# Kernel tuning notes

Measured on AMD Instinct MI355X. Metric: run time of the kernel, lower is better.

Reference implementation:

```python
import jax, jax.numpy as jnp
import numpy as np

N = 8192
FEAT = 3
TRIG = 2
SA = 2
H = 64
ACT = 3
NEG = -1.0e9
EPS = 1e-5


def setup_inputs() -> dict:
    key = jax.random.key(0)
    ks = jax.random.split(key, 24)
    s = 0.05
    node_features = jax.random.uniform(ks[0], (N, FEAT), dtype=jnp.float32)
    adj = jax.random.randint(ks[1], (N, N), 0, 2).astype(jnp.float32)
    # ensure self-loops so every row has at least one neighbor
    adj_matrix = jnp.maximum(adj, jnp.eye(N, dtype=jnp.float32))
    trigger_context = jax.random.uniform(ks[2], (TRIG,), dtype=jnp.float32)
    sa_priors = jax.random.normal(ks[3], (N, SA), dtype=jnp.float32)
    p = lambda k, sh: jax.random.normal(k, sh, dtype=jnp.float32) * s
    return {
        "node_features": node_features,
        "adj_matrix": adj_matrix,
        "trigger_context": trigger_context,
        "sa_priors": sa_priors,
        # node_encoder: Linear(5,64) -> ReLU -> Linear(64,64)
        "w1": p(ks[4], (FEAT + TRIG, H)), "b1": jnp.zeros((H,), jnp.float32),
        "w2": p(ks[5], (H, H)), "b2": jnp.zeros((H,), jnp.float32),
        "wq": p(ks[6], (H, H)), "bq": jnp.zeros((H,), jnp.float32),
        "wk": p(ks[7], (H, H)), "bk": jnp.zeros((H,), jnp.float32),
        "wg": p(ks[8], (TRIG, H)), "bg": jnp.zeros((H,), jnp.float32),
        "stateful_bias": jnp.zeros((1,), jnp.float32),
        "wm": p(ks[9], (H, H)), "bm": jnp.zeros((H,), jnp.float32),
        "ln_g": jnp.ones((H,), jnp.float32), "ln_b": jnp.zeros((H,), jnp.float32),
        "wa1": p(ks[10], (H + SA, H)), "ba1": jnp.zeros((H,), jnp.float32),
        "wa2": p(ks[11], (H, ACT)), "ba2": jnp.zeros((ACT,), jnp.float32),
    }


def reference(node_features, adj_matrix, trigger_context, sa_priors,
              w1, b1, w2, b2, wq, bq, wk, bk, wg, bg, stateful_bias,
              wm, bm, ln_g, ln_b, wa1, ba1, wa2, ba2):
    n = node_features.shape[0]
    trig = jnp.broadcast_to(trigger_context[None, :], (n, TRIG))
    x = jnp.concatenate([node_features, trig], axis=1)          # [N, 5]
    h = jax.nn.relu(x @ w1 + b1) @ w2 + b2                       # [N, H]
    q = h @ wq + bq
    k = h @ wk + bk
    scores = (q @ k.T) * (1.0 / np.sqrt(H))                      # [N, N]
    gate_factor = jnp.mean(jax.nn.sigmoid(trigger_context @ wg + bg))
    topo = jnp.where(adj_matrix == 0, jnp.float32(NEG), adj_matrix)
    is_stateful = node_features[:, 2]
    is_reactive = 1.0 - trigger_context[0]
    sb = jnp.outer(is_stateful, is_stateful) * (stateful_bias[0] * is_reactive)
    scores = scores * gate_factor + topo + sb
    attn = jax.nn.softmax(scores, axis=1)                        # [N, N]
    messages = h @ wm + bm
    aggregated = attn @ messages                                 # [N, H]
    z = h + aggregated
    mu = jnp.mean(z, axis=-1, keepdims=True)
    var = jnp.mean(jnp.square(z - mu), axis=-1, keepdims=True)
    emb = (z - mu) * jax.lax.rsqrt(var + EPS) * ln_g + ln_b      # LayerNorm
    ai = jnp.concatenate([emb, sa_priors], axis=1)               # [N, H+2]
    q_values = jax.nn.relu(ai @ wa1 + ba1) @ wa2 + ba2           # [N, 3]
    return q_values
```

## Files before the change

### kernel.cpp

```cpp
#include <hip/hip_runtime.h>
#include <hip/hip_bf16.h>
#include <math.h>

#define N 8192
#define EPSV 1e-05f
#define NSPLIT 32
#define CPS (N / NSPLIT)
#define NSTEP (CPS / 32)

typedef short bf16x8 __attribute__((ext_vector_type(8)));
typedef float f32x4 __attribute__((ext_vector_type(4)));
typedef float f32x16 __attribute__((ext_vector_type(16)));
typedef unsigned short u16;
typedef unsigned int u32;
typedef unsigned long long u64;

#define WS_SCAL 0
#define WS_H    64
#define WS_ST   (WS_H + N * 64)
#define WS_SBI  (WS_ST + N)
#define WS_DEN  (WS_SBI + N)
#define WS_AGG  (WS_DEN + N)
#define WS_F_END (WS_AGG + N * 64)
#define WU_BASE (WS_F_END * 2)
#define WU_QB (WU_BASE)
#define WU_KB (WU_BASE + N * 64)
#define WU_MB (WU_BASE + 2 * N * 64)
#define WU_MT (WU_BASE + 3 * N * 64)

static __device__ __forceinline__ u16 f2bf(float f) {
    __hip_bfloat16 h = __float2bfloat16(f);
    return *(u16*)&h;
}
static __device__ __forceinline__ u32 pk2(float a, float b) {
    return (u32)f2bf(a) | ((u32)f2bf(b) << 16);
}
static __device__ __forceinline__ bf16x8 mk8(u32 a, u32 b, u32 c, u32 d) {
    union { u32 u[4]; bf16x8 v; } x;
    x.u[0] = a; x.u[1] = b; x.u[2] = c; x.u[3] = d;
    return x.v;
}

__global__ void prep_k(const float* __restrict__ tc, const float* __restrict__ wg,
                       const float* __restrict__ bg, const float* __restrict__ sbias,
                       float* __restrict__ scal) {
    int j = threadIdx.x;
    float v = tc[0] * wg[j] + tc[1] * wg[64 + j] + bg[j];
    float g = 1.0f / (1.0f + __expf(-v));
    for (int off = 32; off; off >>= 1) g += __shfl_xor(g, off, 64);
    if (j == 0) {
        scal[0] = 0.125f * (g * (1.0f / 64.0f));
        scal[1] = sbias[0] * (1.0f - tc[0]);
    }
}

__global__ __launch_bounds__(256) void embed_k(
    const float* __restrict__ nf, const float* __restrict__ tc,
    const float* __restrict__ w1, const float* __restrict__ b1,
    const float* __restrict__ w2, const float* __restrict__ b2,
    const float* __restrict__ wq, const float* __restrict__ bq,
    const float* __restrict__ wk, const float* __restrict__ bk,
    const float* __restrict__ wm, const float* __restrict__ bm,
    float* __restrict__ ws)
{
    const int w = threadIdx.x >> 6, lane = threadIdx.x & 63;
    const int row = blockIdx.x * 4 + w;
    __shared__ float ts[4][64], hs[4][64];
    const float qscale = ws[WS_SCAL + 0];
    const float coef   = ws[WS_SCAL + 1];
    const float f0 = nf[row * 3], f1 = nf[row * 3 + 1], f2 = nf[row * 3 + 2];
    const float t0 = tc[0], t1 = tc[1];
    ws[WS_AGG + (size_t)row * 64 + lane] = 0.0f;
    float v = b1[lane];
    v = fmaf(f0, w1[lane], v);
    v = fmaf(f1, w1[64 + lane], v);
    v = fmaf(f2, w1[128 + lane], v);
    v = fmaf(t0, w1[192 + lane], v);
    v = fmaf(t1, w1[256 + lane], v);
    ts[w][lane] = fmaxf(v, 0.0f);
    __syncthreads();
    float hv = b2[lane];
    #pragma unroll 8
    for (int j = 0; j < 64; j++) hv = fmaf(ts[w][j], w2[j * 64 + lane], hv);
    hs[w][lane] = hv;
    ws[WS_H + row * 64 + lane] = hv;
    __syncthreads();
    float qv = bq[lane], kv = bk[lane], mv = bm[lane];
    #pragma unroll 4
    for (int j = 0; j < 64; j++) {
        const float hj = hs[w][j];
        qv = fmaf(hj, wq[j * 64 + lane], qv);
        kv = fmaf(hj, wk[j * 64 + lane], kv);
        mv = fmaf(hj, wm[j * 64 + lane], mv);
    }
    u16* wu = (u16*)ws;
    wu[WU_QB + row * 64 + lane] = f2bf(qv * qscale);
    wu[WU_KB + row * 64 + lane] = f2bf(kv);
    wu[WU_MB + row * 64 + lane] = f2bf(mv);
    if (lane == 0) {
        ws[WS_ST + row]  = f2;
        ws[WS_SBI + row] = f2 * coef;
        ws[WS_DEN + row] = 0.0f;
    }
}

__global__ __launch_bounds__(256) void transp_k(float* __restrict__ ws) {
    const u16* mb = (const u16*)ws + WU_MB;
    u16* mt = (u16*)ws + WU_MT;
    __shared__ __align__(16) u16 tile[64][72];
    const int i0 = blockIdx.x * 64;
    const int t = threadIdx.x;
    {
        const int r = t >> 2, cb = (t & 3) * 16;
        *(uint4*)&tile[r][cb]     = *(const uint4*)&mb[(size_t)(i0 + r) * 64 + cb];
        *(uint4*)&tile[r][cb + 8] = *(const uint4*)&mb[(size_t)(i0 + r) * 64 + cb + 8];
    }
    __syncthreads();
    const int c = t >> 2, rb = (t & 3) * 16;
    u16 tmp[16];
    #pragma unroll
    for (int i = 0; i < 16; i++) tmp[i] = tile[rb + i][c];
    *(uint4*)&mt[(size_t)c * N + i0 + rb]     = *(uint4*)&tmp[0];
    *(uint4*)&mt[(size_t)c * N + i0 + rb + 8] = *(uint4*)&tmp[8];
}

__global__ __launch_bounds__(512, 4) void attn_k(const float* __restrict__ adj,
                                                 float* __restrict__ ws)
{
    const int rb = blockIdx.x, sp = blockIdx.y;
    const int i0 = rb * 256, j0 = sp * CPS;
    const int tid = threadIdx.x;
    const int w = tid >> 6, lane = tid & 63;
    const int hi = lane >> 5, l31 = lane & 31;

    __shared__ __align__(16) u16 ks[256 * 64];
    __shared__ __align__(16) u16 ms[64 * 256];
    __shared__ u32 abit[256][9];
    __shared__ float stl[CPS];

    const u16* qb  = (const u16*)ws + WU_QB;
    const u16* kbp = (const u16*)ws + WU_KB;
    const u16* mtp = (const u16*)ws + WU_MT;

    {
        const size_t rowbase = (size_t)(i0 + w * 32) * N + j0;
        #pragma unroll 2
        for (int rb8 = 0; rb8 < 4; rb8++) {
            float v[8][4];
            #pragma unroll
            for (int i = 0; i < 8; i++)
                #pragma unroll
                for (int g = 0; g < 4; g++)
                    v[i][g] = adj[rowbase + (size_t)(rb8 * 8 + i) * N + g * 64 + lane];
            #pragma unroll
            for (int i = 0; i < 8; i++) {
                #pragma unroll
                for (int g = 0; g < 4; g++) {
                    const u64 m = __ballot(v[i][g] != 0.0f);
                    if (lane == 0) {
                        abit[w * 32 + rb8 * 8 + i][g * 2]     = (u32)m;
                        abit[w * 32 + rb8 * 8 + i][g * 2 + 1] = (u32)(m >> 32);
                    }
                }
            }
        }
    }

    #pragma unroll
    for (int i = 0; i < 4; i++) {
        const int id = tid + 512 * i;
        const int r = id >> 3, c = id & 7;
        const int off = r * 64 + (((c * 16) ^ ((r & 7) << 4)) >> 1);
        *(uint4*)&ks[off] = *(const uint4*)&kbp[(size_t)(j0 + r) * 64 + c * 8];
    }
    #pragma unroll
    for (int i = 0; i < 4; i++) {
        const int id = tid + 512 * i;
        const int r = id >> 5, c = id & 31;
        const int off = r * 256 + (((c * 16) ^ ((r & 7) << 4)) >> 1);
        *(uint4*)&ms[off] = *(const uint4*)&mtp[(size_t)r * N + j0 + c * 8];
    }
    if (tid < 256) stl[tid] = ws[WS_ST + j0 + tid];
    __syncthreads();

    const int q0 = i0 + w * 32;

    const u16* qr = qb + (size_t)(q0 + l31) * 64;
    bf16x8 qf[4];
    #pragma unroll
    for (int s = 0; s < 4; s++) qf[s] = *(const bf16x8*)&qr[s * 16 + hi * 8];

    const float sbr = ws[WS_SBI + q0 + l31];

    f32x16 acc[2];
    #pragma unroll
    for (int hb = 0; hb < 2; hb++)
        #pragma unroll
        for (int i = 0; i < 16; i++) acc[hb][i] = 0.0f;
    float den = 0.0f;

    #pragma unroll
    for (int s = 0; s < NSTEP; s++) {
        const int loc = s * 32;

        f32x16 d;
        #pragma unroll
        for (int i = 0; i < 16; i++) d[i] = 0.0f;
        __builtin_amdgcn_s_setprio(1);
        #pragma unroll
        for (int s4 = 0; s4 < 4; s4++) {
            const int R = loc + l31;
            const bf16x8 kf = *(const bf16x8*)
                &ks[R * 64 + (((s4 * 32 + hi * 16) ^ ((R & 7) << 4)) >> 1)];
            d = __builtin_amdgcn_mfma_f32_32x32x16_bf16(kf, qf[s4], d, 0, 0, 0);
        }
        __builtin_amdgcn_s_setprio(0);

        const u32 wq = abit[w * 32 + l31][s] >> (4 * hi);

        u32 wlo[4], whi[4];
        #pragma unroll
        for (int c2 = 0; c2 < 4; c2++) {
            const f32x4 sv = *(const f32x4*)&stl[loc + c2 * 8 + hi * 4];
            const float b0 = (float)((wq >> (8 * c2 + 0)) & 1u);
            const float b1 = (float)((wq >> (8 * c2 + 1)) & 1u);
            const float b2 = (float)((wq >> (8 * c2 + 2)) & 1u);
            const float b3 = (float)((wq >> (8 * c2 + 3)) & 1u);
            const float p0 = b0 * __expf(fmaf(sbr, sv[0], d[c2 * 4 + 0]));
            const float p1 = b1 * __expf(fmaf(sbr, sv[1], d[c2 * 4 + 1]));
            const float p2 = b2 * __expf(fmaf(sbr, sv[2], d[c2 * 4 + 2]));
            const float p3 = b3 * __expf(fmaf(sbr, sv[3], d[c2 * 4 + 3]));
            den += (p0 + p1) + (p2 + p3);
            wlo[c2] = pk2(p0, p1);
            whi[c2] = pk2(p2, p3);
        }

        bf16x8 pa[2];
        #pragma unroll
        for (int s2 = 0; s2 < 2; s2++) {
            const u32 xl0 = (u32)__shfl_xor((int)wlo[2 * s2],     32, 64);
            const u32 xh0 = (u32)__shfl_xor((int)whi[2 * s2],     32, 64);
            const u32 xl1 = (u32)__shfl_xor((int)wlo[2 * s2 + 1], 32, 64);
            const u32 xh1 = (u32)__shfl_xor((int)whi[2 * s2 + 1], 32, 64);
            const u32 f0 = hi ? xl1 : wlo[2 * s2];
            const u32 f1 = hi ? xh1 : whi[2 * s2];
            const u32 f2 = hi ? wlo[2 * s2 + 1] : xl0;
            const u32 f3 = hi ? whi[2 * s2 + 1] : xh0;
            pa[s2] = mk8(f0, f1, f2, f3);
        }

        __builtin_amdgcn_s_setprio(1);
        #pragma unroll
        for (int s2 = 0; s2 < 2; s2++) {
            #pragma unroll
            for (int hb = 0; hb < 2; hb++) {
                const int R2 = hb * 32 + l31;
                const bf16x8 mf = *(const bf16x8*)
                    &ms[R2 * 256 +
                        (((loc * 2 + s2 * 32 + hi * 16) ^ ((R2 & 7) << 4)) >> 1)];
                acc[hb] = __builtin_amdgcn_mfma_f32_32x32x16_bf16(pa[s2], mf, acc[hb], 0, 0, 0);
            }
        }
        __builtin_amdgcn_s_setprio(0);
    }

    den += __shfl_xor(den, 32, 64);
    if (hi == 0) unsafeAtomicAdd(&ws[WS_DEN + q0 + l31], den);

    float* aggp = ws + WS_AGG;
    #pragma unroll
    for (int hb = 0; hb < 2; hb++) {
        #pragma unroll
        for (int r = 0; r < 16; r++) {
            const int qv = (r & 3) + 8 * (r >> 2) + 4 * hi;
            unsafeAtomicAdd(&aggp[(size_t)(q0 + qv) * 64 + hb * 32 + l31],
                            acc[hb][r]);
        }
    }
}

__global__ __launch_bounds__(256) void final_k(
    const float* __restrict__ sa, const float* __restrict__ ln_g,
    const float* __restrict__ ln_b,
    const float* __restrict__ wa1, const float* __restrict__ ba1,
    const float* __restrict__ wa2, const float* __restrict__ ba2,
    const float* __restrict__ ws, float* __restrict__ out)
{
    const int w = threadIdx.x >> 6, lane = threadIdx.x & 63;
    const int row = blockIdx.x * 4 + w;
    __shared__ float es[4][64], hs2[4][64];
    const float a = ws[WS_AGG + (size_t)row * 64 + lane];
    const float d = ws[WS_DEN + row];
    const float z = ws[WS_H + row * 64 + lane] + a / d;
    float mu = z;
    for (int off = 32; off; off >>= 1) mu += __shfl_xor(mu, off, 64);
    mu *= (1.0f / 64.0f);
    const float zc = z - mu;
    float var = zc * zc;
    for (int off = 32; off; off >>= 1) var += __shfl_xor(var, off, 64);
    var *= (1.0f / 64.0f);
    const float emb = zc * rsqrtf(var + EPSV) * ln_g[lane] + ln_b[lane];
    es[w][lane] = emb;
    __syncthreads();
    const float sa0 = sa[row * 2], sa1 = sa[row * 2 + 1];
    float hv = ba1[lane];
    #pragma unroll 8
    for (int c = 0; c < 64; c++) hv = fmaf(es[w][c], wa1[c * 64 + lane], hv);
    hv = fmaf(sa0, wa1[64 * 64 + lane], hv);
    hv = fmaf(sa1, wa1[65 * 64 + lane], hv);
    hs2[w][lane] = fmaxf(hv, 0.0f);
    __syncthreads();
    if (lane < 3) {
        float o = ba2[lane];
        for (int u = 0; u < 64; u++) o = fmaf(hs2[w][u], wa2[u * 3 + lane], o);
        out[row * 3 + lane] = o;
    }
}

extern "C" void kernel_launch(void* const* d_in, const int* in_sizes, int n_in,
                              void* d_out, int out_size, void* d_ws, size_t ws_size,
                              hipStream_t stream)
{
    const float* nf  = (const float*)d_in[0];
    const float* adj = (const float*)d_in[1];
    const float* tc  = (const float*)d_in[2];
    const float* sa  = (const float*)d_in[3];
    const float* w1  = (const float*)d_in[4];
    const float* b1  = (const float*)d_in[5];
    const float* w2  = (const float*)d_in[6];
    const float* b2  = (const float*)d_in[7];
    const float* wq  = (const float*)d_in[8];
    const float* bq  = (const float*)d_in[9];
    const float* wk  = (const float*)d_in[10];
    const float* bk  = (const float*)d_in[11];
    const float* wg  = (const float*)d_in[12];
    const float* bg  = (const float*)d_in[13];
    const float* sb  = (const float*)d_in[14];
    const float* wm  = (const float*)d_in[15];
    const float* bm  = (const float*)d_in[16];
    const float* lng = (const float*)d_in[17];
    const float* lnb = (const float*)d_in[18];
    const float* wa1 = (const float*)d_in[19];
    const float* ba1 = (const float*)d_in[20];
    const float* wa2 = (const float*)d_in[21];
    const float* ba2 = (const float*)d_in[22];
    float* ws  = (float*)d_ws;
    float* out = (float*)d_out;

    prep_k<<<1, 64, 0, stream>>>(tc, wg, bg, sb, ws + WS_SCAL);
    embed_k<<<N / 4, 256, 0, stream>>>(nf, tc, w1, b1, w2, b2, wq, bq, wk, bk,
                                       wm, bm, ws);
    transp_k<<<N / 64, 256, 0, stream>>>(ws);
    attn_k<<<dim3(N / 256, NSPLIT), 512, 0, stream>>>(adj, ws);
    final_k<<<N / 4, 256, 0, stream>>>(sa, lng, lnb, wa1, ba1, wa2, ba2, ws, out);
}
```

Before: 450.6 us.

## Precompute adjacency bitmask in separate streaming kernel before attention

Adds a bits_k kernel that reads the dense float adjacency matrix once and packs it into 64-bit nonzero masks in workspace. The attention kernel then loads four mask words per row from global memory instead of reading and ballot-packing its adjacency tile into shared memory. The aim is to move the large adjacency stream into a simple bandwidth-bound pass and shrink the attention kernel's prologue and shared memory. The cost is an extra launch and a global mask round trip, and adjacency loading no longer overlaps with attention compute.

Measured after the change: 501.9 us. 11.4% more time.

```diff
diff --git a/kernel.cpp b/kernel.cpp
--- a/kernel.cpp
+++ b/kernel.cpp
@@ -27,6 +27,8 @@
 #define WU_KB (WU_BASE + N * 64)
 #define WU_MB (WU_BASE + 2 * N * 64)
 #define WU_MT (WU_BASE + 3 * N * 64)
+#define WU_END (WU_BASE + 4 * N * 64)
+#define WB_BYTE ((size_t)WU_END * 2)
 
 static __device__ __forceinline__ u16 f2bf(float f) {
     __hip_bfloat16 h = __float2bfloat16(f);
@@ -52,6 +54,21 @@
         scal[0] = 0.125f * (g * (1.0f / 64.0f));
         scal[1] = sbias[0] * (1.0f - tc[0]);
     }
+}
+
+__global__ __launch_bounds__(256) void bits_k(const float* __restrict__ adj,
+                                              u64* __restrict__ bits) {
+    const int wid = (int)((blockIdx.x * blockDim.x + threadIdx.x) >> 6);
+    const int lane = threadIdx.x & 63;
+    const size_t base = (size_t)wid * 4096;
+    u64 keep = 0;
+    #pragma unroll 16
+    for (int r = 0; r < 64; r++) {
+        const float v = adj[base + (size_t)r * 64 + lane];
+        const u64 m = __ballot(v != 0.0f);
+        if (lane == r) keep = m;
+    }
+    bits[(size_t)wid * 64 + lane] = keep;
 }
 
 __global__ __launch_bounds__(256) void embed_k(
@@ -124,7 +141,7 @@
     *(uint4*)&mt[(size_t)c * N + i0 + rb + 8] = *(uint4*)&tmp[8];
 }
 
-__global__ __launch_bounds__(512, 4) void attn_k(const float* __restrict__ adj,
+__global__ __launch_bounds__(512, 4) void attn_k(const u64* __restrict__ bits,
                                                  float* __restrict__ ws)
 {
     const int rb = blockIdx.x, sp = blockIdx.y;
@@ -135,36 +152,11 @@
 
     __shared__ __align__(16) u16 ks[256 * 64];
     __shared__ __align__(16) u16 ms[64 * 256];
-    __shared__ u32 abit[256][9];
     __shared__ float stl[CPS];
 
     const u16* qb  = (const u16*)ws + WU_QB;
     const u16* kbp = (const u16*)ws + WU_KB;
     const u16* mtp = (const u16*)ws + WU_MT;
-
-    {
-        const size_t rowbase = (size_t)(i0 + w * 32) * N + j0;
-        #pragma unroll 2
-        for (int rb8 = 0; rb8 < 4; rb8++) {
-            float v[8][4];
-            #pragma unroll
-            for (int i = 0; i < 8; i++)
-                #pragma unroll
-                for (int g = 0; g < 4; g++)
-                    v[i][g] = adj[rowbase + (size_t)(rb8 * 8 + i) * N + g * 64 + lane];
-            #pragma unroll
-            for (int i = 0; i < 8; i++) {
-                #pragma unroll
-                for (int g = 0; g < 4; g++) {
-                    const u64 m = __ballot(v[i][g] != 0.0f);
-                    if (lane == 0) {
-                        abit[w * 32 + rb8 * 8 + i][g * 2]     = (u32)m;
-                        abit[w * 32 + rb8 * 8 + i][g * 2 + 1] = (u32)(m >> 32);
-                    }
-                }
-            }
-        }
-    }
 
     #pragma unroll
     for (int i = 0; i < 4; i++) {
@@ -181,9 +173,12 @@
         *(uint4*)&ms[off] = *(const uint4*)&mtp[(size_t)r * N + j0 + c * 8];
     }
     if (tid < 256) stl[tid] = ws[WS_ST + j0 + tid];
-    __syncthreads();
 
     const int q0 = i0 + w * 32;
+
+    const u64* brow = bits + (size_t)(q0 + l31) * (N / 64) + (j0 >> 6);
+    u64 kb[4];
+    kb[0] = brow[0]; kb[1] = brow[1]; kb[2] = brow[2]; kb[3] = brow[3];
 
     const u16* qr = qb + (size_t)(q0 + l31) * 64;
     bf16x8 qf[4];
@@ -191,6 +186,8 @@
     for (int s = 0; s < 4; s++) qf[s] = *(const bf16x8*)&qr[s * 16 + hi * 8];
 
     const float sbr = ws[WS_SBI + q0 + l31];
+
+    __syncthreads();
 
     f32x16 acc[2];
     #pragma unroll
@@ -216,7 +213,8 @@
         }
         __builtin_amdgcn_s_setprio(0);
 
-        const u32 wq = abit[w * 32 + l31][s] >> (4 * hi);
+        const u32 word = (u32)(kb[s >> 1] >> (32 * (s & 1)));
+        const u32 wq = word >> (4 * hi);
 
         u32 wlo[4], whi[4];
         #pragma unroll
@@ -346,11 +344,13 @@
     const float* ba2 = (const float*)d_in[22];
     float* ws  = (float*)d_ws;
     float* out = (float*)d_out;
+    u64* bits = (u64*)((char*)d_ws + WB_BYTE);
 
     prep_k<<<1, 64, 0, stream>>>(tc, wg, bg, sb, ws + WS_SCAL);
+    bits_k<<<(N / 64) * (N / 64) / 4, 256, 0, stream>>>(adj, bits);
     embed_k<<<N / 4, 256, 0, stream>>>(nf, tc, w1, b1, w2, b2, wq, bq, wk, bk,
                                        wm, bm, ws);
     transp_k<<<N / 64, 256, 0, stream>>>(ws);
-    attn_k<<<dim3(N / 256, NSPLIT), 512, 0, stream>>>(adj, ws);
+    attn_k<<<dim3(N / 256, NSPLIT), 512, 0, stream>>>(bits, ws);
     final_k<<<N / 4, 256, 0, stream>>>(sa, lng, lnb, wa1, ba1, wa2, ba2, ws, out);
 }
```
